# Performance work log

Measured on AMD Instinct MI355X. Metric: run time of the kernel, lower is better.

Reference implementation:

```python
import jax, jax.numpy as jnp
import numpy as np

B, S, D = 4, 2048, 1024


def setup_inputs() -> dict:
    key = jax.random.key(0)
    k1, k2, k3, k4 = jax.random.split(key, 4)
    x = jax.random.normal(k1, (B, S, D), dtype=jnp.float32)
    # 'random_normal' keras initializer uses stddev=0.05
    w_keys = jax.random.normal(k2, (D, D), dtype=jnp.float32) * 0.05
    w_queries = jax.random.normal(k3, (D, D), dtype=jnp.float32) * 0.05
    w_values = jax.random.normal(k4, (D, D), dtype=jnp.float32) * 0.05
    return {"x": x, "w_keys": w_keys, "w_queries": w_queries, "w_values": w_values}


def reference(x, w_keys, w_queries, w_values):
    # fact = sqrt(input feature dim)
    fact = jnp.sqrt(jnp.asarray(x.shape[-1], x.dtype))
    vk = x @ w_keys      # [B,S,D]
    vq = x @ w_queries   # [B,S,D]
    vv = x @ w_values    # [B,S,D]
    # NOTE: module computes K @ Q^T (keys as rows), softmax over last axis
    kq = jnp.einsum('bsd,btd->bst', vk, vq) / fact   # [B,S,S]
    sn = jax.nn.softmax(kq, axis=-1)
    # pm + transpose_b cancel: out = sn @ vv
    out = jnp.einsum('bst,btd->bsd', sn, vv)         # [B,S,D]
    return out
```

## Files before the change

### kernel.cpp

```cpp
#include <hip/hip_runtime.h>


typedef __attribute__((ext_vector_type(8))) short bf16x8;
typedef __attribute__((ext_vector_type(4))) float f32x4;

__device__ __forceinline__ unsigned short f2bf(float f) {
    unsigned int u = __float_as_uint(f);
    u += 0x7fff + ((u >> 16) & 1);
    return (unsigned short)(u >> 16);
}

__device__ __forceinline__ void gld_lds16(const unsigned short* g, unsigned short* l) {
    __builtin_amdgcn_global_load_lds(
        (const __attribute__((address_space(1))) void*)g,
        (__attribute__((address_space(3))) void*)l, 16, 0, 0);
}

template<int N> __device__ __forceinline__ void vmcnt_wait() {
    if constexpr (N == 0) asm volatile("s_waitcnt vmcnt(0)" ::: "memory");
    else if constexpr (N == 6) asm volatile("s_waitcnt vmcnt(6)" ::: "memory");
    else if constexpr (N == 8) asm volatile("s_waitcnt vmcnt(8)" ::: "memory");
}

template<int BM, int BN, int KTILES>
__device__ __forceinline__ void gemm_pipe(
    const unsigned short* __restrict__ A, const unsigned short* __restrict__ B,
    int lda, int ldb, int bm, int bn,
    unsigned short* As, unsigned short* Bs,
    f32x4 (&acc)[BM/32][BN/64])
{
    constexpr int LA = BM / 64, LB = BN / 64, L = LA + LB;
    constexpr int MFR = BM / 32, NFR = BN / 64;
    const int tid  = threadIdx.x;
    const int lane = tid & 63;
    const int wave = tid >> 6;
    const int wr = wave >> 2, wc = wave & 3;
    const int lr = lane & 15, kg = lane >> 4;

    const int srow = tid >> 3, su = tid & 7;
    const int ssrc = (su ^ (srow & 7)) * 8;
    const unsigned short* pa[LA];
    const unsigned short* pb[LB];
    #pragma unroll
    for (int i = 0; i < LA; i++) pa[i] = A + (size_t)(bm + i * 64 + srow) * lda + ssrc;
    #pragma unroll
    for (int i = 0; i < LB; i++) pb[i] = B + (size_t)(bn + i * 64 + srow) * ldb + ssrc;

    const int pu0 = (kg ^ (lr & 7)) * 8;
    const int pu1 = ((4 + kg) ^ (lr & 7)) * 8;

    auto stage = [&](int cb, int kt) {
        unsigned short* a0 = As + cb * (BM * 64) + wave * 512;
        unsigned short* b0 = Bs + cb * (BN * 64) + wave * 512;
        #pragma unroll
        for (int i = 0; i < LA; i++) gld_lds16(pa[i] + kt * 64, a0 + i * 4096);
        #pragma unroll
        for (int i = 0; i < LB; i++) gld_lds16(pb[i] + kt * 64, b0 + i * 4096);
    };

    stage(0, 0);
    stage(1, 1);
    vmcnt_wait<L>();
    __builtin_amdgcn_s_barrier();
    asm volatile("" ::: "memory");

    for (int kt = 0; kt < KTILES; ++kt) {
        const int cb = kt & 1;
        const unsigned short* Ab = As + cb * (BM * 64) + (wr * (BM / 2) + lr) * 64;
        const unsigned short* Bb = Bs + cb * (BN * 64) + (wc * (BN / 4) + lr) * 64;

        bf16x8 bfrag[NFR][2];
        #pragma unroll
        for (int nf = 0; nf < NFR; nf++) {
            bfrag[nf][0] = *reinterpret_cast<const bf16x8*>(Bb + nf * 1024 + pu0);
            bfrag[nf][1] = *reinterpret_cast<const bf16x8*>(Bb + nf * 1024 + pu1);
        }
        __builtin_amdgcn_s_setprio(1);
        #pragma unroll
        for (int mf = 0; mf < MFR; mf++) {
            bf16x8 a0 = *reinterpret_cast<const bf16x8*>(Ab + mf * 1024 + pu0);
            bf16x8 a1 = *reinterpret_cast<const bf16x8*>(Ab + mf * 1024 + pu1);
            #pragma unroll
            for (int nf = 0; nf < NFR; nf++) {
                acc[mf][nf] = __builtin_amdgcn_mfma_f32_16x16x32_bf16(a0, bfrag[nf][0], acc[mf][nf], 0, 0, 0);
                acc[mf][nf] = __builtin_amdgcn_mfma_f32_16x16x32_bf16(a1, bfrag[nf][1], acc[mf][nf], 0, 0, 0);
            }
        }
        __builtin_amdgcn_s_setprio(0);

        asm volatile("" ::: "memory");
        __builtin_amdgcn_s_barrier();
        asm volatile("" ::: "memory");
        if (kt + 2 < KTILES) {
            stage(cb, kt + 2);
            vmcnt_wait<L>();
        } else {
            vmcnt_wait<0>();
        }
        __builtin_amdgcn_s_barrier();
        asm volatile("" ::: "memory");
    }
}

__global__ __launch_bounds__(256) void convert_x(
    const float* __restrict__ x, unsigned short* __restrict__ xb)
{
    const size_t idx = (size_t)blockIdx.x * 256 + threadIdx.x;
    const float4* xi = reinterpret_cast<const float4*>(x) + idx * 2;
    float4 v0 = xi[0], v1 = xi[1];
    ushort4 a = { f2bf(v0.x), f2bf(v0.y), f2bf(v0.z), f2bf(v0.w) };
    ushort4 b = { f2bf(v1.x), f2bf(v1.y), f2bf(v1.z), f2bf(v1.w) };
    ushort4* xo = reinterpret_cast<ushort4*>(xb) + idx * 2;
    xo[0] = a; xo[1] = b;
}

__global__ __launch_bounds__(256) void transpose_w(
    const float* __restrict__ w0, const float* __restrict__ w1, const float* __restrict__ w2,
    unsigned short* __restrict__ wT)
{
    __shared__ unsigned short T[64][72];
    const int z = blockIdx.z;
    const float* w = (z == 0) ? w0 : (z == 1 ? w1 : w2);
    unsigned short* o = wT + (size_t)z * 1024 * 1024;
    const int k0 = blockIdx.y * 64, n0 = blockIdx.x * 64;
    const int tid = threadIdx.x;
    const int r = tid >> 4, c4 = (tid & 15) * 4;
    #pragma unroll
    for (int i = 0; i < 4; i++) {
        int kr = r + i * 16;
        float4 v = *reinterpret_cast<const float4*>(&w[(size_t)(k0 + kr) * 1024 + n0 + c4]);
        T[c4 + 0][kr] = f2bf(v.x);
        T[c4 + 1][kr] = f2bf(v.y);
        T[c4 + 2][kr] = f2bf(v.z);
        T[c4 + 3][kr] = f2bf(v.w);
    }
    __syncthreads();
    #pragma unroll
    for (int i = 0; i < 4; i++) {
        int n = r + i * 16;
        ushort4 v = *reinterpret_cast<const ushort4*>(&T[n][c4]);
        *reinterpret_cast<ushort4*>(&o[(size_t)(n0 + n) * 1024 + k0 + c4]) = v;
    }
}

__global__ __launch_bounds__(512, 2) void proj_gemm(
    const unsigned short* __restrict__ xb, const unsigned short* __restrict__ wT,
    unsigned short* __restrict__ vk, unsigned short* __restrict__ vq,
    unsigned short* __restrict__ vvT)
{
    __shared__ unsigned short As[2 * 128 * 64], Bs[2 * 256 * 64];
    const int bid = blockIdx.x;
    const int wg  = (bid & 7) * 96 + (bid >> 3);
    const int z   = wg >> 8;
    const int rem = wg & 255;
    const int bm  = (rem >> 2) * 128;
    const int bn  = (rem & 3) * 256;
    const unsigned short* Bw = wT + (size_t)z * 1024 * 1024;

    f32x4 acc[4][4] = {};
    gemm_pipe<128, 256, 16>(xb, Bw, 1024, 1024, bm, bn, As, Bs, acc);

    const int tid = threadIdx.x, lane = tid & 63, wave = tid >> 6;
    const int wr = wave >> 2, wc = wave & 3, lr = lane & 15, kg = lane >> 4;
    if (z < 2) {
        unsigned short* out = z ? vq : vk;
        #pragma unroll
        for (int mf = 0; mf < 4; mf++)
            #pragma unroll
            for (int nf = 0; nf < 4; nf++)
                #pragma unroll
                for (int r = 0; r < 4; r++)
                    out[(size_t)(bm + wr * 64 + mf * 16 + kg * 4 + r) * 1024
                        + bn + wc * 64 + nf * 16 + lr] = f2bf(acc[mf][nf][r]);
    } else {
        const int batch = bm >> 11;
        const int rb0 = (bm & 2047) + wr * 64;
        unsigned short* o = vvT + (size_t)batch * 1024 * 2048;
        #pragma unroll
        for (int mf = 0; mf < 4; mf++)
            #pragma unroll
            for (int nf = 0; nf < 4; nf++) {
                ushort4 v = { f2bf(acc[mf][nf][0]), f2bf(acc[mf][nf][1]),
                              f2bf(acc[mf][nf][2]), f2bf(acc[mf][nf][3]) };
                *reinterpret_cast<ushort4*>(
                    &o[(size_t)(bn + wc * 64 + nf * 16 + lr) * 2048 + rb0 + mf * 16 + kg * 4]) = v;
            }
    }
}

__global__ __launch_bounds__(512, 2) void scores_gemm(
    const unsigned short* __restrict__ vk, const unsigned short* __restrict__ vq,
    float* __restrict__ scores)
{
    __shared__ unsigned short As[2 * 256 * 64], Bs[2 * 256 * 64];
    const int bid = blockIdx.x;
    const int wg  = (bid & 7) * 32 + (bid >> 3);
    const int z   = wg >> 6;
    const int rem = wg & 63;
    const int bm  = (rem >> 3) * 256;
    const int bn  = (rem & 7) * 256;
    const unsigned short* A = vk + (size_t)z * 2048 * 1024;
    const unsigned short* B = vq + (size_t)z * 2048 * 1024;
    float* out = scores + (size_t)z * 2048 * 2048;

    f32x4 acc[8][4] = {};
    gemm_pipe<256, 256, 16>(A, B, 1024, 1024, bm, bn, As, Bs, acc);

    const int tid = threadIdx.x, lane = tid & 63, wave = tid >> 6;
    const int wr = wave >> 2, wc = wave & 3, lr = lane & 15, kg = lane >> 4;
    #pragma unroll
    for (int mf = 0; mf < 8; mf++)
        #pragma unroll
        for (int nf = 0; nf < 4; nf++)
            #pragma unroll
            for (int r = 0; r < 4; r++)
                out[(size_t)(bm + wr * 128 + mf * 16 + kg * 4 + r) * 2048
                    + bn + wc * 64 + nf * 16 + lr] = acc[mf][nf][r] * 0.03125f;
}

__global__ __launch_bounds__(256) void softmax_kernel(float* __restrict__ scores)
{
    const size_t row = blockIdx.x;
    float* p = scores + row * 2048;
    const int tid  = threadIdx.x;
    const int lane = tid & 63;
    const int wave = tid >> 6;

    float4 v0 = *reinterpret_cast<const float4*>(&p[tid * 8]);
    float4 v1 = *reinterpret_cast<const float4*>(&p[tid * 8 + 4]);
    float v[8] = { v0.x, v0.y, v0.z, v0.w, v1.x, v1.y, v1.z, v1.w };

    float mx = v[0];
    #pragma unroll
    for (int i = 1; i < 8; i++) mx = fmaxf(mx, v[i]);
    #pragma unroll
    for (int off = 32; off >= 1; off >>= 1) mx = fmaxf(mx, __shfl_xor(mx, off));

    __shared__ float redm[4], reds[4];
    if (lane == 0) redm[wave] = mx;
    __syncthreads();
    mx = fmaxf(fmaxf(redm[0], redm[1]), fmaxf(redm[2], redm[3]));

    float e[8], sum = 0.f;
    #pragma unroll
    for (int i = 0; i < 8; i++) { e[i] = __expf(v[i] - mx); sum += e[i]; }
    #pragma unroll
    for (int off = 32; off >= 1; off >>= 1) sum += __shfl_xor(sum, off);
    if (lane == 0) reds[wave] = sum;
    __syncthreads();
    const float inv = 1.0f / (reds[0] + reds[1] + reds[2] + reds[3]);

    unsigned short o[8];
    #pragma unroll
    for (int i = 0; i < 8; i++) o[i] = f2bf(e[i] * inv);
    uint4 packed;
    packed.x = (unsigned)o[0] | ((unsigned)o[1] << 16);
    packed.y = (unsigned)o[2] | ((unsigned)o[3] << 16);
    packed.z = (unsigned)o[4] | ((unsigned)o[5] << 16);
    packed.w = (unsigned)o[6] | ((unsigned)o[7] << 16);
    reinterpret_cast<uint4*>(p)[tid] = packed;
}

__global__ __launch_bounds__(512, 2) void pv_gemm(
    const unsigned short* __restrict__ P, const unsigned short* __restrict__ vvT,
    float* __restrict__ out)
{
    __shared__ unsigned short As[2 * 256 * 64], Bs[2 * 128 * 64];
    const int bid = blockIdx.x;
    const int wg  = (bid & 7) * 32 + (bid >> 3);
    const int z   = wg >> 6;
    const int rem = wg & 63;
    const int bm  = (rem >> 3) * 256;
    const int bn  = (rem & 7) * 128;
    const unsigned short* A = P   + (size_t)z * 2048 * 4096;
    const unsigned short* B = vvT + (size_t)z * 1024 * 2048;
    float* o = out + (size_t)z * 2048 * 1024;

    f32x4 acc[8][2] = {};
    gemm_pipe<256, 128, 32>(A, B, 4096, 2048, bm, bn, As, Bs, acc);

    const int tid = threadIdx.x, lane = tid & 63, wave = tid >> 6;
    const int wr = wave >> 2, wc = wave & 3, lr = lane & 15, kg = lane >> 4;
    #pragma unroll
    for (int mf = 0; mf < 8; mf++)
        #pragma unroll
        for (int nf = 0; nf < 2; nf++)
            #pragma unroll
            for (int r = 0; r < 4; r++)
                o[(size_t)(bm + wr * 128 + mf * 16 + kg * 4 + r) * 1024
                  + bn + wc * 32 + nf * 16 + lr] = acc[mf][nf][r];
}

extern "C" void kernel_launch(void* const* d_in, const int* in_sizes, int n_in,
                              void* d_out, int out_size, void* d_ws, size_t ws_size,
                              hipStream_t stream) {
    const float* x  = (const float*)d_in[0];
    const float* wk = (const float*)d_in[1];
    const float* wq = (const float*)d_in[2];
    const float* wv = (const float*)d_in[3];
    float* out = (float*)d_out;

    char* ws = (char*)d_ws;
    const size_t MB = 1024 * 1024;
    unsigned short* xb  = (unsigned short*)(ws);
    unsigned short* wT  = (unsigned short*)(ws + 16 * MB);
    float*          scores = (float*)(ws);
    unsigned short* vk  = (unsigned short*)(ws + 64 * MB);
    unsigned short* vq  = (unsigned short*)(ws + 80 * MB);
    unsigned short* vvT = (unsigned short*)(ws + 96 * MB);

    convert_x     <<<dim3(4096),      256, 0, stream>>>(x, xb);
    transpose_w   <<<dim3(16, 16, 3), 256, 0, stream>>>(wk, wq, wv, wT);
    proj_gemm     <<<dim3(768),       512, 0, stream>>>(xb, wT, vk, vq, vvT);
    scores_gemm   <<<dim3(256),       512, 0, stream>>>(vk, vq, scores);
    softmax_kernel<<<dim3(8192),      256, 0, stream>>>(scores);
    pv_gemm       <<<dim3(256),       512, 0, stream>>>((const unsigned short*)scores, vvT, out);
}
```

Baseline: 190.1 us.

## Fuse softmax into score and PV GEMMs, restructure pipeline into K-half phases

Removes the standalone softmax kernel. The score GEMM epilogue now writes bf16 exp(score/32) directly, without subtracting the row max. The PV GEMM accumulates row sums from the A fragments it already loads and divides by them in its epilogue. The shared GEMM routine is rewritten to split each K tile into two halves and the N fragments into two groups, overlapping the next tile's async loads with MFMA phases. The projection tiling also changes to 256x128. This removes the fp32 score round trip and one launch. It risks overflow for large logits because there is no max subtraction, and the row sums now come from bf16-rounded values.

Measured after the change: 191.7 us. About the same (+0.8%).

```diff
diff --git a/kernel.cpp b/kernel.cpp
--- a/kernel.cpp
+++ b/kernel.cpp
@@ -9,6 +9,9 @@
     u += 0x7fff + ((u >> 16) & 1);
     return (unsigned short)(u >> 16);
 }
+__device__ __forceinline__ float bf2f(unsigned short s) {
+    return __uint_as_float((unsigned int)s << 16);
+}
 
 __device__ __forceinline__ void gld_lds16(const unsigned short* g, unsigned short* l) {
     __builtin_amdgcn_global_load_lds(
@@ -18,87 +21,132 @@
 
 template<int N> __device__ __forceinline__ void vmcnt_wait() {
     if constexpr (N == 0) asm volatile("s_waitcnt vmcnt(0)" ::: "memory");
-    else if constexpr (N == 6) asm volatile("s_waitcnt vmcnt(6)" ::: "memory");
-    else if constexpr (N == 8) asm volatile("s_waitcnt vmcnt(8)" ::: "memory");
-}
-
-template<int BM, int BN, int KTILES>
-__device__ __forceinline__ void gemm_pipe(
+    else if constexpr (N == 3) asm volatile("s_waitcnt vmcnt(3)" ::: "memory");
+    else if constexpr (N == 4) asm volatile("s_waitcnt vmcnt(4)" ::: "memory");
+}
+__device__ __forceinline__ void bar() {
+    asm volatile("" ::: "memory");
+    __builtin_amdgcn_s_barrier();
+    asm volatile("" ::: "memory");
+}
+
+template<int BN, int KT, bool RS>
+__device__ __forceinline__ void gemm8(
     const unsigned short* __restrict__ A, const unsigned short* __restrict__ B,
     int lda, int ldb, int bm, int bn,
     unsigned short* As, unsigned short* Bs,
-    f32x4 (&acc)[BM/32][BN/64])
-{
-    constexpr int LA = BM / 64, LB = BN / 64, L = LA + LB;
-    constexpr int MFR = BM / 32, NFR = BN / 64;
+    f32x4 (&acc)[8][BN/64], float (&rs)[8])
+{
+    constexpr int NFR = BN / 64, NH = NFR / 2, LB = BN / 128;
     const int tid  = threadIdx.x;
     const int lane = tid & 63;
     const int wave = tid >> 6;
     const int wr = wave >> 2, wc = wave & 3;
     const int lr = lane & 15, kg = lane >> 4;
 
-    const int srow = tid >> 3, su = tid & 7;
-    const int ssrc = (su ^ (srow & 7)) * 8;
-    const unsigned short* pa[LA];
-    const unsigned short* pb[LB];
-    #pragma unroll
-    for (int i = 0; i < LA; i++) pa[i] = A + (size_t)(bm + i * 64 + srow) * lda + ssrc;
-    #pragma unroll
-    for (int i = 0; i < LB; i++) pb[i] = B + (size_t)(bn + i * 64 + srow) * ldb + ssrc;
-
-    const int pu0 = (kg ^ (lr & 7)) * 8;
-    const int pu1 = ((4 + kg) ^ (lr & 7)) * 8;
-
-    auto stage = [&](int cb, int kt) {
-        unsigned short* a0 = As + cb * (BM * 64) + wave * 512;
-        unsigned short* b0 = Bs + cb * (BN * 64) + wave * 512;
-        #pragma unroll
-        for (int i = 0; i < LA; i++) gld_lds16(pa[i] + kt * 64, a0 + i * 4096);
-        #pragma unroll
-        for (int i = 0; i < LB; i++) gld_lds16(pb[i] + kt * 64, b0 + i * 4096);
+    const int srow = tid >> 2;
+    const int soff = ((tid & 3) ^ ((tid >> 3) & 3)) * 8;
+    const unsigned short* pa0 = A + (size_t)(bm + srow) * lda + soff;
+    const unsigned short* pa1 = A + (size_t)(bm + 128 + srow) * lda + soff;
+    const unsigned short* pb0 = B + (size_t)(bn + srow) * ldb + soff;
+    const unsigned short* pb1 = B + (size_t)(bn + 128 + srow) * ldb + soff;
+
+    const int runit = (kg ^ ((lr >> 1) & 3)) * 8;
+    const int arow  = (wr * 128 + lr) * 32 + runit;
+    const int brow  = (wc * (BN / 4) + lr) * 32 + runit;
+
+    auto stageA = [&](int buf, int kt, int kh) {
+        unsigned short* d = As + buf * 16384 + kh * 8192 + wave * 512;
+        const int off = kt * 64 + kh * 32;
+        gld_lds16(pa0 + off, d);
+        gld_lds16(pa1 + off, d + 4096);
     };
-
-    stage(0, 0);
-    stage(1, 1);
-    vmcnt_wait<L>();
-    __builtin_amdgcn_s_barrier();
-    asm volatile("" ::: "memory");
-
-    for (int kt = 0; kt < KTILES; ++kt) {
-        const int cb = kt & 1;
-        const unsigned short* Ab = As + cb * (BM * 64) + (wr * (BM / 2) + lr) * 64;
-        const unsigned short* Bb = Bs + cb * (BN * 64) + (wc * (BN / 4) + lr) * 64;
-
-        bf16x8 bfrag[NFR][2];
-        #pragma unroll
-        for (int nf = 0; nf < NFR; nf++) {
-            bfrag[nf][0] = *reinterpret_cast<const bf16x8*>(Bb + nf * 1024 + pu0);
-            bfrag[nf][1] = *reinterpret_cast<const bf16x8*>(Bb + nf * 1024 + pu1);
+    auto stageB = [&](int buf, int kt, int kh) {
+        unsigned short* d = Bs + buf * (BN * 64) + kh * (BN * 32) + wave * 512;
+        const int off = kt * 64 + kh * 32;
+        gld_lds16(pb0 + off, d);
+        if constexpr (BN == 256) gld_lds16(pb1 + off, d + 4096);
+    };
+
+    stageA(0, 0, 0); stageB(0, 0, 0); stageA(0, 0, 1); stageB(0, 0, 1);
+    vmcnt_wait<0>();
+    bar();
+
+    for (int kt = 0; kt < KT; ++kt) {
+        const int c = kt & 1, n = c ^ 1;
+        const bool last = (kt == KT - 1);
+        const unsigned short* Ab = As + c * 16384 + arow;
+        const unsigned short* Bb = Bs + c * (BN * 64) + brow;
+
+        bf16x8 af[8], bfr[NH];
+        #pragma unroll
+        for (int mf = 0; mf < 8; mf++) af[mf] = *reinterpret_cast<const bf16x8*>(Ab + mf * 512);
+        #pragma unroll
+        for (int j = 0; j < NH; j++) bfr[j] = *reinterpret_cast<const bf16x8*>(Bb + j * 512);
+        if (!last) stageA(n, kt + 1, 0);
+        bar();
+        __builtin_amdgcn_s_setprio(1);
+        #pragma unroll
+        for (int mf = 0; mf < 8; mf++)
+            #pragma unroll
+            for (int j = 0; j < NH; j++)
+                acc[mf][j] = __builtin_amdgcn_mfma_f32_16x16x32_bf16(af[mf], bfr[j], acc[mf][j], 0, 0, 0);
+        __builtin_amdgcn_s_setprio(0);
+        if constexpr (RS) {
+            #pragma unroll
+            for (int mf = 0; mf < 8; mf++)
+                #pragma unroll
+                for (int e = 0; e < 8; e++) rs[mf] += bf2f(((unsigned short*)&af[mf])[e]);
         }
+        bar();
+
+        #pragma unroll
+        for (int j = 0; j < NH; j++) bfr[j] = *reinterpret_cast<const bf16x8*>(Bb + (NH + j) * 512);
+        if (!last) stageB(n, kt + 1, 0);
+        if (last) vmcnt_wait<0>(); else vmcnt_wait<2 + LB>();
+        bar();
         __builtin_amdgcn_s_setprio(1);
         #pragma unroll
-        for (int mf = 0; mf < MFR; mf++) {
-            bf16x8 a0 = *reinterpret_cast<const bf16x8*>(Ab + mf * 1024 + pu0);
-            bf16x8 a1 = *reinterpret_cast<const bf16x8*>(Ab + mf * 1024 + pu1);
-            #pragma unroll
-            for (int nf = 0; nf < NFR; nf++) {
-                acc[mf][nf] = __builtin_amdgcn_mfma_f32_16x16x32_bf16(a0, bfrag[nf][0], acc[mf][nf], 0, 0, 0);
-                acc[mf][nf] = __builtin_amdgcn_mfma_f32_16x16x32_bf16(a1, bfrag[nf][1], acc[mf][nf], 0, 0, 0);
-            }
+        for (int mf = 0; mf < 8; mf++)
+            #pragma unroll
+            for (int j = 0; j < NH; j++)
+                acc[mf][NH + j] = __builtin_amdgcn_mfma_f32_16x16x32_bf16(af[mf], bfr[j], acc[mf][NH + j], 0, 0, 0);
+        __builtin_amdgcn_s_setprio(0);
+        bar();
+
+        #pragma unroll
+        for (int mf = 0; mf < 8; mf++) af[mf] = *reinterpret_cast<const bf16x8*>(Ab + 8192 + mf * 512);
+        #pragma unroll
+        for (int j = 0; j < NH; j++) bfr[j] = *reinterpret_cast<const bf16x8*>(Bb + BN * 32 + j * 512);
+        if (!last) stageA(n, kt + 1, 1);
+        bar();
+        __builtin_amdgcn_s_setprio(1);
+        #pragma unroll
+        for (int mf = 0; mf < 8; mf++)
+            #pragma unroll
+            for (int j = 0; j < NH; j++)
+                acc[mf][j] = __builtin_amdgcn_mfma_f32_16x16x32_bf16(af[mf], bfr[j], acc[mf][j], 0, 0, 0);
+        __builtin_amdgcn_s_setprio(0);
+        if constexpr (RS) {
+            #pragma unroll
+            for (int mf = 0; mf < 8; mf++)
+                #pragma unroll
+                for (int e = 0; e < 8; e++) rs[mf] += bf2f(((unsigned short*)&af[mf])[e]);
         }
+        bar();
+
+        #pragma unroll
+        for (int j = 0; j < NH; j++) bfr[j] = *reinterpret_cast<const bf16x8*>(Bb + BN * 32 + (NH + j) * 512);
+        if (!last) { stageB(n, kt + 1, 1); vmcnt_wait<2 + LB>(); }
+        bar();
+        __builtin_amdgcn_s_setprio(1);
+        #pragma unroll
+        for (int mf = 0; mf < 8; mf++)
+            #pragma unroll
+            for (int j = 0; j < NH; j++)
+                acc[mf][NH + j] = __builtin_amdgcn_mfma_f32_16x16x32_bf16(af[mf], bfr[j], acc[mf][NH + j], 0, 0, 0);
         __builtin_amdgcn_s_setprio(0);
-
-        asm volatile("" ::: "memory");
-        __builtin_amdgcn_s_barrier();
-        asm volatile("" ::: "memory");
-        if (kt + 2 < KTILES) {
-            stage(cb, kt + 2);
-            vmcnt_wait<L>();
-        } else {
-            vmcnt_wait<0>();
-        }
-        __builtin_amdgcn_s_barrier();
-        asm volatile("" ::: "memory");
+        bar();
     }
 }
 
@@ -148,49 +196,50 @@
     unsigned short* __restrict__ vk, unsigned short* __restrict__ vq,
     unsigned short* __restrict__ vvT)
 {
-    __shared__ unsigned short As[2 * 128 * 64], Bs[2 * 256 * 64];
+    __shared__ unsigned short As[2 * 256 * 64], Bs[2 * 128 * 64];
     const int bid = blockIdx.x;
     const int wg  = (bid & 7) * 96 + (bid >> 3);
     const int z   = wg >> 8;
     const int rem = wg & 255;
-    const int bm  = (rem >> 2) * 128;
-    const int bn  = (rem & 3) * 256;
+    const int bm  = (rem >> 3) * 256;
+    const int bn  = (rem & 7) * 128;
     const unsigned short* Bw = wT + (size_t)z * 1024 * 1024;
 
-    f32x4 acc[4][4] = {};
-    gemm_pipe<128, 256, 16>(xb, Bw, 1024, 1024, bm, bn, As, Bs, acc);
+    f32x4 acc[8][2] = {};
+    float rs[8] = {};
+    gemm8<128, 16, false>(xb, Bw, 1024, 1024, bm, bn, As, Bs, acc, rs);
 
     const int tid = threadIdx.x, lane = tid & 63, wave = tid >> 6;
     const int wr = wave >> 2, wc = wave & 3, lr = lane & 15, kg = lane >> 4;
     if (z < 2) {
         unsigned short* out = z ? vq : vk;
         #pragma unroll
-        for (int mf = 0; mf < 4; mf++)
-            #pragma unroll
-            for (int nf = 0; nf < 4; nf++)
+        for (int mf = 0; mf < 8; mf++)
+            #pragma unroll
+            for (int nf = 0; nf < 2; nf++)
                 #pragma unroll
                 for (int r = 0; r < 4; r++)
-                    out[(size_t)(bm + wr * 64 + mf * 16 + kg * 4 + r) * 1024
-                        + bn + wc * 64 + nf * 16 + lr] = f2bf(acc[mf][nf][r]);
+                    out[(size_t)(bm + wr * 128 + mf * 16 + kg * 4 + r) * 1024
+                        + bn + wc * 32 + nf * 16 + lr] = f2bf(acc[mf][nf][r]);
     } else {
         const int batch = bm >> 11;
-        const int rb0 = (bm & 2047) + wr * 64;
         unsigned short* o = vvT + (size_t)batch * 1024 * 2048;
         #pragma unroll
-        for (int mf = 0; mf < 4; mf++)
-            #pragma unroll
-            for (int nf = 0; nf < 4; nf++) {
+        for (int mf = 0; mf < 8; mf++)
+            #pragma unroll
+            for (int nf = 0; nf < 2; nf++) {
                 ushort4 v = { f2bf(acc[mf][nf][0]), f2bf(acc[mf][nf][1]),
                               f2bf(acc[mf][nf][2]), f2bf(acc[mf][nf][3]) };
                 *reinterpret_cast<ushort4*>(
-                    &o[(size_t)(bn + wc * 64 + nf * 16 + lr) * 2048 + rb0 + mf * 16 + kg * 4]) = v;
+                    &o[(size_t)(bn + wc * 32 + nf * 16 + lr) * 2048
+                       + (bm & 2047) + wr * 128 + mf * 16 + kg * 4]) = v;
             }
     }
 }
 
 __global__ __launch_bounds__(512, 2) void scores_gemm(
     const unsigned short* __restrict__ vk, const unsigned short* __restrict__ vq,
-    float* __restrict__ scores)
+    unsigned short* __restrict__ P)
 {
     __shared__ unsigned short As[2 * 256 * 64], Bs[2 * 256 * 64];
     const int bid = blockIdx.x;
@@ -201,10 +250,11 @@
     const int bn  = (rem & 7) * 256;
     const unsigned short* A = vk + (size_t)z * 2048 * 1024;
     const unsigned short* B = vq + (size_t)z * 2048 * 1024;
-    float* out = scores + (size_t)z * 2048 * 2048;
+    unsigned short* out = P + (size_t)z * 2048 * 2048;
 
     f32x4 acc[8][4] = {};
-    gemm_pipe<256, 256, 16>(A, B, 1024, 1024, bm, bn, As, Bs, acc);
+    float rs[8] = {};
+    gemm8<256, 16, false>(A, B, 1024, 1024, bm, bn, As, Bs, acc, rs);
 
     const int tid = threadIdx.x, lane = tid & 63, wave = tid >> 6;
     const int wr = wave >> 2, wc = wave & 3, lr = lane & 15, kg = lane >> 4;
@@ -215,50 +265,8 @@
             #pragma unroll
             for (int r = 0; r < 4; r++)
                 out[(size_t)(bm + wr * 128 + mf * 16 + kg * 4 + r) * 2048
-                    + bn + wc * 64 + nf * 16 + lr] = acc[mf][nf][r] * 0.03125f;
-}
-
-__global__ __launch_bounds__(256) void softmax_kernel(float* __restrict__ scores)
-{
-    const size_t row = blockIdx.x;
-    float* p = scores + row * 2048;
-    const int tid  = threadIdx.x;
-    const int lane = tid & 63;
-    const int wave = tid >> 6;
-
-    float4 v0 = *reinterpret_cast<const float4*>(&p[tid * 8]);
-    float4 v1 = *reinterpret_cast<const float4*>(&p[tid * 8 + 4]);
-    float v[8] = { v0.x, v0.y, v0.z, v0.w, v1.x, v1.y, v1.z, v1.w };
-
-    float mx = v[0];
-    #pragma unroll
-    for (int i = 1; i < 8; i++) mx = fmaxf(mx, v[i]);
-    #pragma unroll
-    for (int off = 32; off >= 1; off >>= 1) mx = fmaxf(mx, __shfl_xor(mx, off));
-
-    __shared__ float redm[4], reds[4];
-    if (lane == 0) redm[wave] = mx;
-    __syncthreads();
-    mx = fmaxf(fmaxf(redm[0], redm[1]), fmaxf(redm[2], redm[3]));
-
-    float e[8], sum = 0.f;
-    #pragma unroll
-    for (int i = 0; i < 8; i++) { e[i] = __expf(v[i] - mx); sum += e[i]; }
-    #pragma unroll
-    for (int off = 32; off >= 1; off >>= 1) sum += __shfl_xor(sum, off);
-    if (lane == 0) reds[wave] = sum;
-    __syncthreads();
-    const float inv = 1.0f / (reds[0] + reds[1] + reds[2] + reds[3]);
-
-    unsigned short o[8];
-    #pragma unroll
-    for (int i = 0; i < 8; i++) o[i] = f2bf(e[i] * inv);
-    uint4 packed;
-    packed.x = (unsigned)o[0] | ((unsigned)o[1] << 16);
-    packed.y = (unsigned)o[2] | ((unsigned)o[3] << 16);
-    packed.z = (unsigned)o[4] | ((unsigned)o[5] << 16);
-    packed.w = (unsigned)o[6] | ((unsigned)o[7] << 16);
-    reinterpret_cast<uint4*>(p)[tid] = packed;
+                    + bn + wc * 64 + nf * 16 + lr]
+                    = f2bf(__expf(acc[mf][nf][r] * 0.03125f));
 }
 
 __global__ __launch_bounds__(512, 2) void pv_gemm(
@@ -272,23 +280,33 @@
     const int rem = wg & 63;
     const int bm  = (rem >> 3) * 256;
     const int bn  = (rem & 7) * 128;
-    const unsigned short* A = P   + (size_t)z * 2048 * 4096;
+    const unsigned short* A = P   + (size_t)z * 2048 * 2048;
     const unsigned short* B = vvT + (size_t)z * 1024 * 2048;
     float* o = out + (size_t)z * 2048 * 1024;
 
     f32x4 acc[8][2] = {};
-    gemm_pipe<256, 128, 32>(A, B, 4096, 2048, bm, bn, As, Bs, acc);
+    float rs[8] = {};
+    gemm8<128, 32, true>(A, B, 2048, 2048, bm, bn, As, Bs, acc, rs);
 
     const int tid = threadIdx.x, lane = tid & 63, wave = tid >> 6;
     const int wr = wave >> 2, wc = wave & 3, lr = lane & 15, kg = lane >> 4;
+
+    #pragma unroll
+    for (int mf = 0; mf < 8; mf++) {
+        rs[mf] += __shfl_xor(rs[mf], 16);
+        rs[mf] += __shfl_xor(rs[mf], 32);
+    }
     #pragma unroll
     for (int mf = 0; mf < 8; mf++)
         #pragma unroll
-        for (int nf = 0; nf < 2; nf++)
-            #pragma unroll
-            for (int r = 0; r < 4; r++)
+        for (int r = 0; r < 4; r++) {
+            const float l = __shfl(rs[mf], kg * 4 + r);
+            const float inv = 1.0f / l;
+            #pragma unroll
+            for (int nf = 0; nf < 2; nf++)
                 o[(size_t)(bm + wr * 128 + mf * 16 + kg * 4 + r) * 1024
-                  + bn + wc * 32 + nf * 16 + lr] = acc[mf][nf][r];
+                  + bn + wc * 32 + nf * 16 + lr] = acc[mf][nf][r] * inv;
+        }
 }
 
 extern "C" void kernel_launch(void* const* d_in, const int* in_sizes, int n_in,
@@ -304,15 +322,14 @@
     const size_t MB = 1024 * 1024;
     unsigned short* xb  = (unsigned short*)(ws);
     unsigned short* wT  = (unsigned short*)(ws + 16 * MB);
-    float*          scores = (float*)(ws);
+    unsigned short* P   = (unsigned short*)(ws);
     unsigned short* vk  = (unsigned short*)(ws + 64 * MB);
     unsigned short* vq  = (unsigned short*)(ws + 80 * MB);
     unsigned short* vvT = (unsigned short*)(ws + 96 * MB);
 
-    convert_x     <<<dim3(4096),      256, 0, stream>>>(x, xb);
-    transpose_w   <<<dim3(16, 16, 3), 256, 0, stream>>>(wk, wq, wv, wT);
-    proj_gemm     <<<dim3(768),       512, 0, stream>>>(xb, wT, vk, vq, vvT);
-    scores_gemm   <<<dim3(256),       512, 0, stream>>>(vk, vq, scores);
-    softmax_kernel<<<dim3(8192),      256, 0, stream>>>(scores);
-    pv_gemm       <<<dim3(256),       512, 0, stream>>>((const unsigned short*)scores, vvT, out);
-}
+    convert_x  <<<dim3(4096),      256, 0, stream>>>(x, xb);
+    transpose_w<<<dim3(16, 16, 3), 256, 0, stream>>>(wk, wq, wv, wT);
+    proj_gemm  <<<dim3(768),       512, 0, stream>>>(xb, wT, vk, vq, vvT);
+    scores_gemm<<<dim3(256),       512, 0, stream>>>(vk, vq, P);
+    pv_gemm    <<<dim3(256),       512, 0, stream>>>(P, vvT, out);
+}
```
